# Optimization experiments

Measured on AMD Instinct MI355X. Metric: run time of the kernel, lower is better.

The kernel has to match this reference:

```python
import jax, jax.numpy as jnp
import numpy as np

# Config (matches init_kwargs)
B, N, F, S, T, L = 4, 128, 128, 5, 32, 2
R_MAX = 10.0
AVG_NEI = 16.0
# ell index of each of the 16 spherical-harmonic components (l=0..3)
ELL_IDX = np.array([0] + [1]*3 + [2]*5 + [3]*7)


def _edges(n):
    # fully-connected directed edge list without self loops (static)
    i = np.arange(n)
    s = np.repeat(i, n)
    r = np.tile(i, n)
    m = s != r
    return jnp.asarray(s[m]), jnp.asarray(r[m])


def _sh(u):
    # real spherical harmonics up to ell=3, component normalization, unit input
    x, y, z = u[..., 0], u[..., 1], u[..., 2]
    s3, s5, s15 = 3**0.5, 5**0.5, 15**0.5
    s35_8, s105, s21_8, s7 = (35/8)**0.5, 105**0.5, (21/8)**0.5, 7**0.5
    comps = [jnp.ones_like(x),
             s3*x, s3*y, s3*z,
             s15*x*y, s15*y*z, 0.5*s5*(3*z*z - 1), s15*x*z, 0.5*s15*(x*x - y*y),
             s35_8*y*(3*x*x - y*y), s105*x*y*z, s21_8*y*(5*z*z - 1),
             0.5*s7*z*(5*z*z - 3), s21_8*x*(5*z*z - 1),
             0.5*s105*z*(x*x - y*y), s35_8*x*(x*x - 3*y*y)]
    return jnp.stack(comps, axis=-1)  # (E,16)


def _forward(positions, node_features, global_features, W_embed, b_embed,
             Wr1, br1, Wr2, Wnode, c1, c2, c3, Wmix0, Wmix1, Wg1, Wg2, Wvout):
    n = positions.shape[1]
    senders, receivers = _edges(n)
    ell = jnp.asarray(ELL_IDX)

    def single(pos, nf, te):
        pos0 = pos
        node_attrs = jax.nn.one_hot(nf - 1, S, dtype=pos.dtype)
        h = jnp.concatenate([node_attrs, jnp.tile(te, (n, 1))], axis=-1)
        scal = h @ W_embed + b_embed            # (N,F) scalar node feats
        vec = jnp.zeros((n, F, 3), pos.dtype)   # (N,F,3) vector node feats
        v = pos[receivers] - pos[senders]       # (E,3)
        lng = jnp.sqrt(jnp.sum(v*v, -1, keepdims=True) + 1e-12)  # (E,1)
        env = 0.5*(jnp.cos(jnp.pi*lng/R_MAX) + 1.0)*(lng < R_MAX)  # cutoff from lengths_0
        for i in range(L):
            u = v / lng
            Y = _sh(u)                                            # (E,16)
            Rw = jax.nn.silu(lng @ Wr1[i] + br1[i]) @ Wr2[i]      # radial MLP (E,4F)
            Rw = (Rw * env).reshape(-1, 4, F)                     # (E,4,F)
            z = (scal @ Wnode[i])[senders]                        # (E,F)
            vdot = jnp.einsum('ecd,ed->ec', vec[senders], u)      # (E,F)
            f = z + vdot
            # tensor-product messages (E,16,F)
            M = Rw[:, ell, :] * Y[:, :, None] * f[:, None, :]
            A = jnp.zeros((n, 16, F), pos.dtype).at[receivers].add(M) / AVG_NEI
            # correlation-3 symmetric-contraction gate via per-ell invariants
            nrm = jnp.zeros((n, 4, F), pos.dtype).at[:, ell, :].add(A*A)
            g = 1.0 + c1[i]*nrm + c2[i]*nrm*nrm + c3[i]*nrm*nrm*nrm
            A = A * g[:, ell, :]
            # linear mix to hidden irreps 128x0e + 128x1o
            scal = A[:, 0, :] @ Wmix0[i]                          # (N,F)
            vec = jnp.einsum('nmc,ck->nkm', A[:, 1:4, :], Wmix1[i])  # (N,F,3)
            # nonlinear readout -> equivariant position update
            gate = jax.nn.silu(scal @ Wg1[i]) @ Wg2[i]            # (N,F)
            mbv = jnp.sum(vec * (gate * Wvout[i])[:, :, None], 1) # (N,3)
            pos = pos + mbv
            v = pos[receivers] - pos[senders]
            lng = jnp.sqrt(jnp.sum(v*v, -1, keepdims=True) + 1e-12)
        return pos - pos0  # predicted noise on positions

    return jax.vmap(single)(positions, node_features, global_features)


def setup_inputs() -> dict:
    key = jax.random.key(0)
    ks = jax.random.split(key, 20)
    sc = 0.1
    p = {}
    p['positions'] = jax.random.normal(ks[0], (B, N, 3), jnp.float32)
    p['node_features'] = jax.random.randint(ks[1], (B, N), 1, S + 1).astype(jnp.int32)
    p['global_features'] = jax.random.normal(ks[2], (B, T), jnp.float32)
    p['W_embed'] = jax.random.normal(ks[3], (S + T, F)) * sc
    p['b_embed'] = jnp.zeros((F,))
    p['Wr1'] = jax.random.normal(ks[4], (L, 1, 64)) * sc
    p['br1'] = jnp.zeros((L, 64))
    p['Wr2'] = jax.random.normal(ks[5], (L, 64, 4 * F)) * sc
    p['Wnode'] = jax.random.normal(ks[6], (L, F, F)) * sc
    p['c1'] = jax.random.normal(ks[7], (L, 4, F)) * 0.01
    p['c2'] = jax.random.normal(ks[8], (L, 4, F)) * 0.001
    p['c3'] = jax.random.normal(ks[9], (L, 4, F)) * 0.0001
    p['Wmix0'] = jax.random.normal(ks[10], (L, F, F)) * sc
    p['Wmix1'] = jax.random.normal(ks[11], (L, F, F)) * sc
    p['Wg1'] = jax.random.normal(ks[12], (L, F, 16)) * sc
    p['Wg2'] = jax.random.normal(ks[13], (L, 16, F)) * sc
    p['Wvout'] = jax.random.normal(ks[14], (L, F)) * sc
    return p


def reference(positions, node_features, global_features, W_embed, b_embed,
              Wr1, br1, Wr2, Wnode, c1, c2, c3, Wmix0, Wmix1, Wg1, Wg2, Wvout):
    return _forward(positions, node_features, global_features, W_embed, b_embed,
                    Wr1, br1, Wr2, Wnode, c1, c2, c3, Wmix0, Wmix1, Wg1, Wg2, Wvout)
```

## Files before the change

### kernel.cpp

```cpp
#include <hip/hip_runtime.h>
#include <hip/hip_bf16.h>
#include <math.h>

#define NB 4
#define NN 128
#define NF 128
#define NS 5
#define NT 32
#define NL 2

typedef __hip_bfloat16 bf16;
typedef short bf16x8 __attribute__((ext_vector_type(8)));
typedef float f32x4 __attribute__((ext_vector_type(4)));

__device__ __forceinline__ float b2f(const bf16 x) { return __bfloat162float(x); }
__device__ __forceinline__ float fast_rcp(float x) { return __builtin_amdgcn_rcpf(x); }
__device__ __forceinline__ float fast_rsq(float x) { return __builtin_amdgcn_rsqf(x); }
__device__ __forceinline__ float silu_fast(float x) { return x * fast_rcp(1.0f + __expf(-x)); }
__device__ __forceinline__ float ldf(const void* p, int i, int fl) {
  return fl ? b2f(((const bf16*)p)[i]) : ((const float*)p)[i];
}
__device__ __forceinline__ short f2bf(float x) {
  unsigned u = __float_as_uint(x);
  unsigned r = (u + 0x7fffu + ((u >> 16) & 1u)) >> 16;
  return (short)r;
}

#define PI_F 3.14159265358979323846f
#define SQRT3_F 1.7320508075688772f

#define POS_OFF 0
#define GF_OFF  1536
#define WE_OFF  1664
#define BE_OFF  6400
#define WR1_OFF 6528
#define BR1_OFF 6656
#define WR2_OFF 6784
#define WN_OFF  72320
#define C1_OFF  105088
#define C2_OFF  106112
#define C3_OFF  107136
#define M0_OFF  108160
#define M1_OFF  140928
#define G1_OFF  173696
#define G2_OFF  177792
#define WV_OFF  181888
#define CVT_TOTAL 182144

__global__ void prep_convert_kernel(
    const void* __restrict__ pos_raw, const int* __restrict__ nfeat,
    const void* __restrict__ gf,  const void* __restrict__ we,
    const void* __restrict__ be,  const void* __restrict__ wr1,
    const void* __restrict__ br1, const void* __restrict__ wr2,
    const void* __restrict__ wn,  const void* __restrict__ c1,
    const void* __restrict__ c2,  const void* __restrict__ c3,
    const void* __restrict__ m0,  const void* __restrict__ m1,
    const void* __restrict__ g1,  const void* __restrict__ g2,
    const void* __restrict__ wv,
    int* __restrict__ flag, float* __restrict__ cvt,
    float* __restrict__ pos_cur, float* __restrict__ z,
    float* __restrict__ env, short* __restrict__ pkw)
{
  __shared__ float posB[NN*3];
  __shared__ float scs[NF];
  __shared__ int sbad;
  const int tid = threadIdx.x;
  const int bn  = blockIdx.x;
  const int b   = bn >> 7;
  const int n   = bn & 127;

  if (tid == 0) sbad = 0;
  __syncthreads();
  {
    const bf16* p = (const bf16*)pos_raw;
    int bad = 0;
    for (int i = tid; i < NB*NN*3; i += 256) {
      float v = b2f(p[i]);
      if (!(fabsf(v) <= 1024.0f)) bad = 1;
    }
    if (bad) sbad = 1;
  }
  __syncthreads();
  const int fl = sbad ? 0 : 1;
  if (bn == 0 && tid == 0) *flag = fl;

  for (int i = bn*256 + tid; i < CVT_TOTAL; i += 512*256) {
    const void* src; int j;
    if      (i < GF_OFF)  { src = pos_raw; j = i - POS_OFF; }
    else if (i < WE_OFF)  { src = gf;  j = i - GF_OFF; }
    else if (i < BE_OFF)  { src = we;  j = i - WE_OFF; }
    else if (i < WR1_OFF) { src = be;  j = i - BE_OFF; }
    else if (i < BR1_OFF) { src = wr1; j = i - WR1_OFF; }
    else if (i < WN_OFF)  { src = br1; j = i - BR1_OFF; }
    else if (i < C1_OFF)  { src = wr2; j = i - WR2_OFF; }
    else if (i < C2_OFF)  { src = c1;  j = i - C1_OFF; }
    else if (i < C3_OFF)  { src = c2;  j = i - C2_OFF; }
    else if (i < M0_OFF)  { src = c3;  j = i - C3_OFF; }
    else if (i < M1_OFF)  { src = m0;  j = i - M0_OFF; }
    else if (i < G1_OFF)  { src = m1;  j = i - M1_OFF; }
    else if (i < G2_OFF)  { src = g1;  j = i - G1_OFF; }
    else if (i < WV_OFF)  { src = g2;  j = i - G2_OFF; }
    else                  { src = wv;  j = i - WV_OFF; }
    if (i < WN_OFF && i >= C1_OFF) { }
    if      (i >= WN_OFF && i < C1_OFF) { src = wn; j = i - WN_OFF; }
    cvt[i] = fl ? b2f(((const bf16*)src)[j]) : ((const float*)src)[j];
  }

  if (bn < 16) {
    int gid  = bn*256 + tid;
    int lyr  = gid >> 11;
    int r    = gid & 2047;
    int wv2  = r >> 9;
    int t    = (r >> 7) & 3;
    int ks   = (r >> 6) & 1;
    int lane = r & 63;
    int qq = lane >> 4, nn = lane & 15;
    int col = wv2*64 + t*16 + nn;
    short* dst = pkw + (size_t)gid*8;
    #pragma unroll
    for (int j = 0; j < 8; ++j) {
      int k = ks*32 + qq*8 + j;
      float v = ldf(wr2, lyr*64*512 + k*512 + col, fl);
      if (wv2 >= 2) v *= SQRT3_F;
      dst[j] = f2bf(v);
    }
  }

  for (int i = tid; i < NN*3; i += 256)
    posB[i] = ldf(pos_raw, b*NN*3 + i, fl);
  if (tid < 128) {
    int sp = nfeat[bn] - 1;
    float acc = ldf(we, sp*NF + tid, fl) + ldf(be, tid, fl);
    #pragma unroll 8
    for (int t = 0; t < NT; ++t)
      acc += ldf(gf, b*NT + t, fl) * ldf(we, (NS + t)*NF + tid, fl);
    scs[tid] = acc;
  }
  __syncthreads();

  if (tid < 128) {
    const int f = tid;
    {
      float px = posB[n*3+0], py = posB[n*3+1], pz = posB[n*3+2];
      float vx = px - posB[f*3+0];
      float vy = py - posB[f*3+1];
      float vz = pz - posB[f*3+2];
      float lng = sqrtf(vx*vx + vy*vy + vz*vz + 1e-12f);
      env[bn*NN + f] = (lng < 10.0f) ? 0.5f*(cosf(PI_F*lng*0.1f) + 1.0f) : 0.0f;
    }
    {
      float acc = 0.f;
      if (fl) {
        const bf16* W = (const bf16*)wn;
        #pragma unroll 8
        for (int k = 0; k < NF; ++k) acc += scs[k] * b2f(W[k*NF + f]);
      } else {
        const float* W = (const float*)wn;
        #pragma unroll 8
        for (int k = 0; k < NF; ++k) acc += scs[k] * W[k*NF + f];
      }
      z[bn*NF + f] = acc;
    }
    if (f < 3) pos_cur[bn*3 + f] = posB[n*3 + f];
  }
}

__global__ __launch_bounds__(256, 2)
void fused_kernel(const float* __restrict__ posIn, float* __restrict__ posOut,
                  const float* __restrict__ zIn,  float* __restrict__ zOut,
                  const float* __restrict__ vecIn, float* __restrict__ vecOut,
                  const float* __restrict__ env,  const float* __restrict__ cvt,
                  const short* __restrict__ pk, int layer, int last,
                  const int* __restrict__ flag, void* __restrict__ out)
{
  union SM {
    float4 zvp[2][16][NF];
    struct {
      float P[8][32][17];
      float Pg[8][16];
      float scs[NF];
      float h16[16];
      float red[2][4];
    } nd;
  };
  __shared__ __align__(16) SM sm;
  __shared__ float posL[NN*3];
  __shared__ float envL[NN];
  __shared__ float w1L[64], b1L[64];
  __shared__ __align__(16) short hidA[2][16][72];
  __shared__ __align__(16) float4 uenvL[2][16];
  __shared__ float Ash[4][NF];

  const int tid  = threadIdx.x;
  const int bidx = blockIdx.x;
  const int b    = bidx >> 7;
  const int n    = bidx & 127;

  const int wvid  = tid >> 6;
  const int lane  = tid & 63;
  const int n16   = lane & 15;
  const int q     = lane >> 4;
  const int halfB = wvid >> 1;

  for (int i = tid; i < NN*3; i += 256)
    posL[i] = posIn[b*NN*3 + i];
  if (tid < 128) envL[tid] = env[(size_t)(b*NN + n)*NN + tid];
  if (tid < 64) {
    w1L[tid] = cvt[WR1_OFF + layer*64 + tid];
    b1L[tid] = cvt[BR1_OFF + layer*64 + tid];
  }
  bf16x8 bfr[4][2];
  {
    const bf16x8* PK = (const bf16x8*)pk + (size_t)layer*2048 + wvid*512 + lane;
    #pragma unroll
    for (int t = 0; t < 4; ++t) {
      #pragma unroll
      for (int ks = 0; ks < 2; ++ks)
        bfr[t][ks] = PK[(t*2 + ks)*64];
    }
  }
  float acR[12];
  #pragma unroll
  for (int i = 0; i < 12; ++i) acR[i] = 0.f;

  __syncthreads();

  const float hrx = posL[n*3 + 0];
  const float hry = posL[n*3 + 1];
  const float hrz = posL[n*3 + 2];
  const float w1v = w1L[lane], b1v = b1L[lane];

  const int fS  = tid & 127;
  const int si0 = tid >> 7;

  float4 pv[8];

  #pragma unroll
  for (int rep = 0; rep < 8; ++rep) {
    int sl = si0 + 2*rep;
    int gs = b*NN + sl;
    pv[rep].x = zIn[gs*NF + fS];
    if (layer) {
      pv[rep].y = vecIn[((size_t)gs*3 + 0)*NF + fS];
      pv[rep].z = vecIn[((size_t)gs*3 + 1)*NF + fS];
      pv[rep].w = vecIn[((size_t)gs*3 + 2)*NF + fS];
    } else { pv[rep].y = 0.f; pv[rep].z = 0.f; pv[rep].w = 0.f; }
  }
  #pragma unroll
  for (int j = 0; j < 4; ++j) {
    int si = wvid*4 + j;
    int s  = si;
    float vx = hrx - posL[s*3 + 0];
    float vy = hry - posL[s*3 + 1];
    float vz = hrz - posL[s*3 + 2];
    float d = vx*vx + vy*vy + vz*vz + 1e-12f;
    float lng = d * fast_rsq(d);
    hidA[0][si][lane] = f2bf(silu_fast(lng * w1v + b1v));
  }
  if (tid < 16) {
    int s = tid;
    float vx = hrx - posL[s*3 + 0];
    float vy = hry - posL[s*3 + 1];
    float vz = hrz - posL[s*3 + 2];
    float d = vx*vx + vy*vy + vz*vz + 1e-12f;
    float inv = fast_rsq(d);
    float envw = (s == n) ? 0.f : envL[s] * 0.0625f;
    uenvL[0][tid] = make_float4(vx*inv, vy*inv, vz*inv, envw);
  }
  #pragma unroll
  for (int rep = 0; rep < 8; ++rep)
    sm.zvp[0][si0 + 2*rep][fS] = pv[rep];
  __syncthreads();

  #pragma unroll 2
  for (int c = 0; c < 8; ++c) {
    const int cb = c & 1, nb = cb ^ 1;
    const int nc0 = (c + 1) * 16;

    if (c < 7) {
      #pragma unroll
      for (int rep = 0; rep < 8; ++rep) {
        int gs = b*NN + nc0 + si0 + 2*rep;
        pv[rep].x = zIn[gs*NF + fS];
        if (layer) {
          pv[rep].y = vecIn[((size_t)gs*3 + 0)*NF + fS];
          pv[rep].z = vecIn[((size_t)gs*3 + 1)*NF + fS];
          pv[rep].w = vecIn[((size_t)gs*3 + 2)*NF + fS];
        } else { pv[rep].y = 0.f; pv[rep].z = 0.f; pv[rep].w = 0.f; }
      }
    }

    bf16x8 af0 = *(const bf16x8*)&hidA[cb][n16][q*8];
    bf16x8 af1 = *(const bf16x8*)&hidA[cb][n16][q*8 + 32];
    float4 ue[4];
    #pragma unroll
    for (int r = 0; r < 4; ++r) ue[r] = uenvL[cb][q*4 + r];

    #pragma unroll
    for (int t = 0; t < 4; ++t) {
      f32x4 Cf = {0.f, 0.f, 0.f, 0.f};
      Cf = __builtin_amdgcn_mfma_f32_16x16x32_bf16(af0, bfr[t][0], Cf, 0, 0, 0);
      Cf = __builtin_amdgcn_mfma_f32_16x16x32_bf16(af1, bfr[t][1], Cf, 0, 0, 0);
      int f = (wvid*64 + t*16 + n16) & 127;
      if (!halfB) {
        float a0 = 0.f;
        #pragma unroll
        for (int r = 0; r < 4; ++r) {
          float4 zv = sm.zvp[cb][q*4 + r][f];
          float fv = zv.x + ue[r].x*zv.y + ue[r].y*zv.z + ue[r].z*zv.w;
          a0 += (Cf[r] * ue[r].w) * fv;
        }
        acR[t] += a0;
      } else {
        float t1 = 0.f, t2 = 0.f, t3 = 0.f;
        #pragma unroll
        for (int r = 0; r < 4; ++r) {
          float4 zv = sm.zvp[cb][q*4 + r][f];
          float fv = zv.x + ue[r].x*zv.y + ue[r].y*zv.z + ue[r].z*zv.w;
          float tt = (Cf[r] * ue[r].w) * fv;
          t1 += tt * ue[r].x;
          t2 += tt * ue[r].y;
          t3 += tt * ue[r].z;
        }
        acR[t*3 + 0] += t1;
        acR[t*3 + 1] += t2;
        acR[t*3 + 2] += t3;
      }
    }

    if (c < 7) {
      #pragma unroll
      for (int j = 0; j < 4; ++j) {
        int si = wvid*4 + j;
        int s  = nc0 + si;
        float vx = hrx - posL[s*3 + 0];
        float vy = hry - posL[s*3 + 1];
        float vz = hrz - posL[s*3 + 2];
        float d = vx*vx + vy*vy + vz*vz + 1e-12f;
        float lng = d * fast_rsq(d);
        hidA[nb][si][lane] = f2bf(silu_fast(lng * w1v + b1v));
      }
      if (tid < 16) {
        int s = nc0 + tid;
        float vx = hrx - posL[s*3 + 0];
        float vy = hry - posL[s*3 + 1];
        float vz = hrz - posL[s*3 + 2];
        float d = vx*vx + vy*vy + vz*vz + 1e-12f;
        float inv = fast_rsq(d);
        float envw = (s == n) ? 0.f : envL[s] * 0.0625f;
        uenvL[nb][tid] = make_float4(vx*inv, vy*inv, vz*inv, envw);
      }
      #pragma unroll
      for (int rep = 0; rep < 8; ++rep)
        sm.zvp[nb][si0 + 2*rep][fS] = pv[rep];
    }
    __syncthreads();
  }

  #pragma unroll
  for (int i = 0; i < 12; ++i) {
    float v = acR[i];
    v += __shfl_xor(v, 16, 64);
    v += __shfl_xor(v, 32, 64);
    acR[i] = v;
  }
  if (lane < 16) {
    #pragma unroll
    for (int t = 0; t < 4; ++t) {
      int f = (wvid*64 + t*16 + lane) & 127;
      if (!halfB) {
        Ash[0][f] = acR[t];
      } else {
        Ash[1][f] = acR[t*3 + 0];
        Ash[2][f] = acR[t*3 + 1];
        Ash[3][f] = acR[t*3 + 2];
      }
    }
  }
  __syncthreads();

  const int fn = tid & 127;
  float v0 = 0.f, v1 = 0.f, v2 = 0.f;

  if (tid < 128) {
    float a0 = Ash[0][fn];
    float a1 = Ash[1][fn];
    float a2 = Ash[2][fn];
    float a3 = Ash[3][fn];
    float n0 = a0*a0;
    float C1 = cvt[C1_OFF + (layer*4 + 0)*NF + fn];
    float C2 = cvt[C2_OFF + (layer*4 + 0)*NF + fn];
    float C3 = cvt[C3_OFF + (layer*4 + 0)*NF + fn];
    float g0 = 1.0f + C1*n0 + C2*n0*n0 + C3*n0*n0*n0;
    float n1 = a1*a1 + a2*a2 + a3*a3;
    float D1 = cvt[C1_OFF + (layer*4 + 1)*NF + fn];
    float D2 = cvt[C2_OFF + (layer*4 + 1)*NF + fn];
    float D3 = cvt[C3_OFF + (layer*4 + 1)*NF + fn];
    float g1 = 1.0f + D1*n1 + D2*n1*n1 + D3*n1*n1*n1;
    Ash[0][fn] = a0 * g0;
    Ash[1][fn] = a1 * g1;
    Ash[2][fn] = a2 * g1;
    Ash[3][fn] = a3 * g1;
  }
  __syncthreads();

  {
    const float* M0 = cvt + M0_OFF + layer*NF*NF;
    const float* M1 = cvt + M1_OFF + layer*NF*NF;
    const int kh = tid >> 5;
    const int fq = tid & 31;
    float s0=0.f,s1=0.f,s2=0.f,s3=0.f;
    float w00=0.f,w01=0.f,w02=0.f,w03=0.f;
    float w10=0.f,w11=0.f,w12=0.f,w13=0.f;
    float w20=0.f,w21=0.f,w22=0.f,w23=0.f;
    #pragma unroll 4
    for (int kk = 0; kk < 16; ++kk) {
      int k = kh*16 + kk;
      float a0 = Ash[0][k], a1 = Ash[1][k], a2 = Ash[2][k], a3 = Ash[3][k];
      float4 m0 = *(const float4*)(M0 + k*NF + fq*4);
      float4 m1 = *(const float4*)(M1 + k*NF + fq*4);
      s0 += a0*m0.x; s1 += a0*m0.y; s2 += a0*m0.z; s3 += a0*m0.w;
      w00 += a1*m1.x; w01 += a1*m1.y; w02 += a1*m1.z; w03 += a1*m1.w;
      w10 += a2*m1.x; w11 += a2*m1.y; w12 += a2*m1.z; w13 += a2*m1.w;
      w20 += a3*m1.x; w21 += a3*m1.y; w22 += a3*m1.z; w23 += a3*m1.w;
    }
    float* Pp = &sm.nd.P[kh][fq][0];
    Pp[0]=s0;  Pp[1]=s1;  Pp[2]=s2;  Pp[3]=s3;
    Pp[4]=w00; Pp[5]=w01; Pp[6]=w02; Pp[7]=w03;
    Pp[8]=w10; Pp[9]=w11; Pp[10]=w12; Pp[11]=w13;
    Pp[12]=w20; Pp[13]=w21; Pp[14]=w22; Pp[15]=w23;
  }
  __syncthreads();

  if (tid < 128) {
    int fq = fn >> 2, j = fn & 3;
    float sn = 0.f;
    #pragma unroll
    for (int kh = 0; kh < 8; ++kh) {
      const float* Pp = &sm.nd.P[kh][fq][0];
      sn += Pp[j];
      v0 += Pp[4 + j];
      v1 += Pp[8 + j];
      v2 += Pp[12 + j];
    }
    sm.nd.scs[fn] = sn;
  }
  __syncthreads();

  if (!last) {
    const float* W = cvt + WN_OFF + (layer+1)*NF*NF;
    const int kh = tid >> 5;
    const int fq = tid & 31;
    float s0=0.f,s1=0.f,s2=0.f,s3=0.f;
    #pragma unroll 4
    for (int kk = 0; kk < 16; ++kk) {
      int k = kh*16 + kk;
      float a = sm.nd.scs[k];
      float4 m = *(const float4*)(W + k*NF + fq*4);
      s0 += a*m.x; s1 += a*m.y; s2 += a*m.z; s3 += a*m.w;
    }
    float* Pp = &sm.nd.P[kh][fq][0];
    Pp[0]=s0; Pp[1]=s1; Pp[2]=s2; Pp[3]=s3;
  }
  if (tid < 128) {
    const float* G1 = cvt + G1_OFF + layer*NF*16;
    int o = tid & 15, g = tid >> 4;
    float acc = 0.f;
    #pragma unroll
    for (int kk = 0; kk < 16; ++kk) {
      int k = g*16 + kk;
      acc += sm.nd.scs[k] * G1[k*16 + o];
    }
    sm.nd.Pg[g][o] = acc;
  }
  __syncthreads();

  if (!last && tid < 128) {
    int fq = fn >> 2, j = fn & 3;
    float acc = 0.f;
    #pragma unroll
    for (int kh = 0; kh < 8; ++kh) acc += sm.nd.P[kh][fq][j];
    zOut[bidx*NF + fn] = acc;
  }
  if (tid < 16) {
    float acc = 0.f;
    #pragma unroll
    for (int g = 0; g < 8; ++g) acc += sm.nd.Pg[g][tid];
    sm.nd.h16[tid] = silu_fast(acc);
  }
  __syncthreads();

  if (tid < 128) {
    const float* G2 = cvt + G2_OFF + layer*16*NF;
    float gate = 0.f;
    #pragma unroll
    for (int j = 0; j < 16; ++j)
      gate += sm.nd.h16[j] * G2[j*NF + fn];
    float gv = gate * cvt[WV_OFF + layer*NF + fn];

    if (!last) {
      vecOut[((size_t)bidx*3 + 0)*NF + fn] = v0;
      vecOut[((size_t)bidx*3 + 1)*NF + fn] = v1;
      vecOut[((size_t)bidx*3 + 2)*NF + fn] = v2;
    }

    float p0 = v0*gv, p1 = v1*gv, p2 = v2*gv;
    #pragma unroll
    for (int off = 32; off > 0; off >>= 1) {
      p0 += __shfl_down(p0, off, 64);
      p1 += __shfl_down(p1, off, 64);
      p2 += __shfl_down(p2, off, 64);
    }
    int wave = fn >> 6;
    if ((fn & 63) == 0) {
      sm.nd.red[wave][0] = p0;
      sm.nd.red[wave][1] = p1;
      sm.nd.red[wave][2] = p2;
    }
  }
  __syncthreads();
  if (tid == 0) {
    float m0 = sm.nd.red[0][0] + sm.nd.red[1][0];
    float m1 = sm.nd.red[0][1] + sm.nd.red[1][1];
    float m2 = sm.nd.red[0][2] + sm.nd.red[1][2];
    float px = posL[n*3+0] + m0;
    float py = posL[n*3+1] + m1;
    float pz = posL[n*3+2] + m2;
    if (!last) {
      posOut[bidx*3+0] = px;
      posOut[bidx*3+1] = py;
      posOut[bidx*3+2] = pz;
    } else {
      float ox = px - cvt[POS_OFF + bidx*3+0];
      float oy = py - cvt[POS_OFF + bidx*3+1];
      float oz = pz - cvt[POS_OFF + bidx*3+2];
      if (*flag) {
        bf16* o = (bf16*)out;
        o[bidx*3+0] = __float2bfloat16(ox);
        o[bidx*3+1] = __float2bfloat16(oy);
        o[bidx*3+2] = __float2bfloat16(oz);
      } else {
        float* o = (float*)out;
        o[bidx*3+0] = ox;
        o[bidx*3+1] = oy;
        o[bidx*3+2] = oz;
      }
    }
  }
}

extern "C" void kernel_launch(void* const* d_in, const int* in_sizes, int n_in,
                              void* d_out, int out_size, void* d_ws, size_t ws_size,
                              hipStream_t stream)
{
  (void)in_sizes; (void)n_in; (void)out_size; (void)ws_size;
  const int* nfeat = (const int*)d_in[1];

  float* ws   = (float*)d_ws;
  int*   flag = (int*)ws;
  float* cvt  = ws + 16;
  float* pos0 = cvt + CVT_TOTAL;
  float* pos1 = pos0 + NB*NN*3;
  float* z0   = pos1 + NB*NN*3;
  float* z1   = z0 + NB*NN*NF;
  float* vec1 = z1 + NB*NN*NF;
  float* env  = vec1 + NB*NN*3*NF;
  short* pk   = (short*)(env + NB*NN*NN);

  prep_convert_kernel<<<512, 256, 0, stream>>>(
      d_in[0], nfeat, d_in[2], d_in[3], d_in[4], d_in[5], d_in[6], d_in[7],
      d_in[8], d_in[9], d_in[10], d_in[11], d_in[12], d_in[13], d_in[14],
      d_in[15], d_in[16], flag, cvt, pos0, z0, env, pk);

  fused_kernel<<<512, 256, 0, stream>>>(pos0, pos1, z0, z1, (const float*)0,
                                        vec1, env, cvt, pk, 0, 0, flag, d_out);
  fused_kernel<<<512, 256, 0, stream>>>(pos1, (float*)0, z1, (float*)0, vec1,
                                        (float*)0, env, cvt, pk, 1, 1, flag, d_out);
}
```

Before: 145.9 us.

## Interleave z and vec into float4 buffer and stream tiles via global_load_lds

```diff
diff --git a/kernel.cpp b/kernel.cpp
--- a/kernel.cpp
+++ b/kernel.cpp
@@ -12,6 +12,9 @@
 typedef __hip_bfloat16 bf16;
 typedef short bf16x8 __attribute__((ext_vector_type(8)));
 typedef float f32x4 __attribute__((ext_vector_type(4)));
+
+typedef const void __attribute__((address_space(1))) gv_t;
+typedef void __attribute__((address_space(3))) lv_t;
 
 __device__ __forceinline__ float b2f(const bf16 x) { return __bfloat162float(x); }
 __device__ __forceinline__ float fast_rcp(float x) { return __builtin_amdgcn_rcpf(x); }
@@ -24,6 +27,9 @@
   unsigned u = __float_as_uint(x);
   unsigned r = (u + 0x7fffu + ((u >> 16) & 1u)) >> 16;
   return (short)r;
+}
+__device__ __forceinline__ void gload16(const float4* g, float4* l) {
+  __builtin_amdgcn_global_load_lds((gv_t*)g, (lv_t*)l, 16, 0, 0);
 }
 
 #define PI_F 3.14159265358979323846f
@@ -58,7 +64,7 @@
     const void* __restrict__ g1,  const void* __restrict__ g2,
     const void* __restrict__ wv,
     int* __restrict__ flag, float* __restrict__ cvt,
-    float* __restrict__ pos_cur, float* __restrict__ z,
+    float* __restrict__ pos_cur, float4* __restrict__ zv,
     float* __restrict__ env, short* __restrict__ pkw)
 {
   __shared__ float posB[NN*3];
@@ -91,8 +97,9 @@
     else if (i < BE_OFF)  { src = we;  j = i - WE_OFF; }
     else if (i < WR1_OFF) { src = be;  j = i - BE_OFF; }
     else if (i < BR1_OFF) { src = wr1; j = i - WR1_OFF; }
-    else if (i < WN_OFF)  { src = br1; j = i - BR1_OFF; }
-    else if (i < C1_OFF)  { src = wr2; j = i - WR2_OFF; }
+    else if (i < WR2_OFF) { src = br1; j = i - BR1_OFF; }
+    else if (i < WN_OFF)  { src = wr2; j = i - WR2_OFF; }
+    else if (i < C1_OFF)  { src = wn;  j = i - WN_OFF; }
     else if (i < C2_OFF)  { src = c1;  j = i - C1_OFF; }
     else if (i < C3_OFF)  { src = c2;  j = i - C2_OFF; }
     else if (i < M0_OFF)  { src = c3;  j = i - C3_OFF; }
@@ -101,8 +108,6 @@
     else if (i < G2_OFF)  { src = g1;  j = i - G1_OFF; }
     else if (i < WV_OFF)  { src = g2;  j = i - G2_OFF; }
     else                  { src = wv;  j = i - WV_OFF; }
-    if (i < WN_OFF && i >= C1_OFF) { }
-    if      (i >= WN_OFF && i < C1_OFF) { src = wn; j = i - WN_OFF; }
     cvt[i] = fl ? b2f(((const bf16*)src)[j]) : ((const float*)src)[j];
   }
 
@@ -159,7 +164,7 @@
         #pragma unroll 8
         for (int k = 0; k < NF; ++k) acc += scs[k] * W[k*NF + f];
       }
-      z[bn*NF + f] = acc;
+      zv[(size_t)bn*NF + f] = make_float4(acc, 0.f, 0.f, 0.f);
     }
     if (f < 3) pos_cur[bn*3 + f] = posB[n*3 + f];
   }
@@ -167,8 +172,7 @@
 
 __global__ __launch_bounds__(256, 2)
 void fused_kernel(const float* __restrict__ posIn, float* __restrict__ posOut,
-                  const float* __restrict__ zIn,  float* __restrict__ zOut,
-                  const float* __restrict__ vecIn, float* __restrict__ vecOut,
+                  const float4* __restrict__ zvIn, float4* __restrict__ zvOut,
                   const float* __restrict__ env,  const float* __restrict__ cvt,
                   const short* __restrict__ pk, int layer, int last,
                   const int* __restrict__ flag, void* __restrict__ out)
@@ -202,6 +206,14 @@
   const int q     = lane >> 4;
   const int halfB = wvid >> 1;
 
+  {
+    const float4* g = zvIn + (size_t)b*NN*NF + wvid*64 + lane;
+    float4* l = &sm.zvp[0][0][0] + wvid*64;
+    #pragma unroll
+    for (int rep = 0; rep < 8; ++rep)
+      gload16(g + rep*256, l + rep*256);
+  }
+
   for (int i = tid; i < NN*3; i += 256)
     posL[i] = posIn[b*NN*3 + i];
   if (tid < 128) envL[tid] = env[(size_t)(b*NN + n)*NN + tid];
@@ -230,22 +242,6 @@
   const float hrz = posL[n*3 + 2];
   const float w1v = w1L[lane], b1v = b1L[lane];
 
-  const int fS  = tid & 127;
-  const int si0 = tid >> 7;
-
-  float4 pv[8];
-
-  #pragma unroll
-  for (int rep = 0; rep < 8; ++rep) {
-    int sl = si0 + 2*rep;
-    int gs = b*NN + sl;
-    pv[rep].x = zIn[gs*NF + fS];
-    if (layer) {
-      pv[rep].y = vecIn[((size_t)gs*3 + 0)*NF + fS];
-      pv[rep].z = vecIn[((size_t)gs*3 + 1)*NF + fS];
-      pv[rep].w = vecIn[((size_t)gs*3 + 2)*NF + fS];
-    } else { pv[rep].y = 0.f; pv[rep].z = 0.f; pv[rep].w = 0.f; }
-  }
   #pragma unroll
   for (int j = 0; j < 4; ++j) {
     int si = wvid*4 + j;
@@ -267,9 +263,6 @@
     float envw = (s == n) ? 0.f : envL[s] * 0.0625f;
     uenvL[0][tid] = make_float4(vx*inv, vy*inv, vz*inv, envw);
   }
-  #pragma unroll
-  for (int rep = 0; rep < 8; ++rep)
-    sm.zvp[0][si0 + 2*rep][fS] = pv[rep];
   __syncthreads();
 
   #pragma unroll 2
@@ -278,16 +271,11 @@
     const int nc0 = (c + 1) * 16;
 
     if (c < 7) {
+      const float4* g = zvIn + ((size_t)b*NN + nc0)*NF + wvid*64 + lane;
+      float4* l = &sm.zvp[nb][0][0] + wvid*64;
       #pragma unroll
-      for (int rep = 0; rep < 8; ++rep) {
-        int gs = b*NN + nc0 + si0 + 2*rep;
-        pv[rep].x = zIn[gs*NF + fS];
-        if (layer) {
-          pv[rep].y = vecIn[((size_t)gs*3 + 0)*NF + fS];
-          pv[rep].z = vecIn[((size_t)gs*3 + 1)*NF + fS];
-          pv[rep].w = vecIn[((size_t)gs*3 + 2)*NF + fS];
-        } else { pv[rep].y = 0.f; pv[rep].z = 0.f; pv[rep].w = 0.f; }
-      }
+      for (int rep = 0; rep < 8; ++rep)
+        gload16(g + rep*256, l + rep*256);
     }
 
     bf16x8 af0 = *(const bf16x8*)&hidA[cb][n16][q*8];
@@ -350,9 +338,6 @@
         float envw = (s == n) ? 0.f : envL[s] * 0.0625f;
         uenvL[nb][tid] = make_float4(vx*inv, vy*inv, vz*inv, envw);
       }
-      #pragma unroll
-      for (int rep = 0; rep < 8; ++rep)
-        sm.zvp[nb][si0 + 2*rep][fS] = pv[rep];
     }
     __syncthreads();
   }
@@ -381,6 +366,7 @@
 
   const int fn = tid & 127;
   float v0 = 0.f, v1 = 0.f, v2 = 0.f;
+  float zacc = 0.f;
 
   if (tid < 128) {
     float a0 = Ash[0][fn];
@@ -477,10 +463,8 @@
 
   if (!last && tid < 128) {
     int fq = fn >> 2, j = fn & 3;
-    float acc = 0.f;
-    #pragma unroll
-    for (int kh = 0; kh < 8; ++kh) acc += sm.nd.P[kh][fq][j];
-    zOut[bidx*NF + fn] = acc;
+    #pragma unroll
+    for (int kh = 0; kh < 8; ++kh) zacc += sm.nd.P[kh][fq][j];
   }
   if (tid < 16) {
     float acc = 0.f;
@@ -498,11 +482,8 @@
       gate += sm.nd.h16[j] * G2[j*NF + fn];
     float gv = gate * cvt[WV_OFF + layer*NF + fn];
 
-    if (!last) {
-      vecOut[((size_t)bidx*3 + 0)*NF + fn] = v0;
-      vecOut[((size_t)bidx*3 + 1)*NF + fn] = v1;
-      vecOut[((size_t)bidx*3 + 2)*NF + fn] = v2;
-    }
+    if (!last)
+      zvOut[(size_t)bidx*NF + fn] = make_float4(zacc, v0, v1, v2);
 
     float p0 = v0*gv, p1 = v1*gv, p2 = v2*gv;
     #pragma unroll
@@ -556,24 +537,23 @@
   (void)in_sizes; (void)n_in; (void)out_size; (void)ws_size;
   const int* nfeat = (const int*)d_in[1];
 
-  float* ws   = (float*)d_ws;
-  int*   flag = (int*)ws;
-  float* cvt  = ws + 16;
-  float* pos0 = cvt + CVT_TOTAL;
-  float* pos1 = pos0 + NB*NN*3;
-  float* z0   = pos1 + NB*NN*3;
-  float* z1   = z0 + NB*NN*NF;
-  float* vec1 = z1 + NB*NN*NF;
-  float* env  = vec1 + NB*NN*3*NF;
-  short* pk   = (short*)(env + NB*NN*NN);
+  float*  ws   = (float*)d_ws;
+  int*    flag = (int*)ws;
+  float*  cvt  = ws + 16;
+  float*  pos0 = cvt + CVT_TOTAL;
+  float*  pos1 = pos0 + NB*NN*3;
+  float4* zv0  = (float4*)(pos1 + NB*NN*3);
+  float4* zv1  = zv0 + (size_t)NB*NN*NF;
+  float*  env  = (float*)(zv1 + (size_t)NB*NN*NF);
+  short*  pk   = (short*)(env + NB*NN*NN);
 
   prep_convert_kernel<<<512, 256, 0, stream>>>(
       d_in[0], nfeat, d_in[2], d_in[3], d_in[4], d_in[5], d_in[6], d_in[7],
       d_in[8], d_in[9], d_in[10], d_in[11], d_in[12], d_in[13], d_in[14],
-      d_in[15], d_in[16], flag, cvt, pos0, z0, env, pk);
-
-  fused_kernel<<<512, 256, 0, stream>>>(pos0, pos1, z0, z1, (const float*)0,
-                                        vec1, env, cvt, pk, 0, 0, flag, d_out);
-  fused_kernel<<<512, 256, 0, stream>>>(pos1, (float*)0, z1, (float*)0, vec1,
-                                        (float*)0, env, cvt, pk, 1, 1, flag, d_out);
+      d_in[15], d_in[16], flag, cvt, pos0, zv0, env, pk);
+
+  fused_kernel<<<512, 256, 0, stream>>>(pos0, pos1, zv0, zv1, env, cvt, pk,
+                                        0, 0, flag, d_out);
+  fused_kernel<<<512, 256, 0, stream>>>(pos1, (float*)0, zv1, (float4*)0, env,
+                                        cvt, pk, 1, 1, flag, d_out);
 }
```

Result: faster. 141.8 us (-2.8%).
